# Performance work log

Hardware: AMD Instinct MI355X
Metric: run time of the kernel (lower is better)

## Reference

```python
import jax, jax.numpy as jnp
import numpy as np

B, N, DESC, H, MAXK = 32, 2048, 16, 64, 2
P = DESC + H            # concat feature dim
KMAT = 2 * MAXK + 1     # num diffusion matrices (identity + MAXK per support)


def setup_inputs() -> dict:
    key = jax.random.key(0)
    ks = jax.random.split(key, 8)
    return {
        "inputs": jax.random.normal(ks[0], (B, N * DESC), jnp.float32),
        "state": jax.random.normal(ks[1], (B, N * H), jnp.float32),
        "adj": jax.random.uniform(ks[2], (N, N), jnp.float32),
        "theta_r": jax.random.normal(ks[3], (P * KMAT, H), jnp.float32) * 0.05,
        "theta_u": jax.random.normal(ks[4], (P * KMAT, H), jnp.float32) * 0.05,
        "theta_c": jax.random.normal(ks[5], (P * KMAT, H), jnp.float32) * 0.05,
        "bias_r": jnp.zeros((1, H), jnp.float32),
        "bias_u": jnp.zeros((1, H), jnp.float32),
        "bias_c": jnp.zeros((1, H), jnp.float32),
    }


def _random_walk_T(adj):
    # transpose(D^-1 A): row-normalize then transpose
    d = jnp.sum(adj, axis=1, keepdims=True)
    d_inv = jnp.where(d > 0, 1.0 / d, 0.0)
    return (d_inv * adj).T  # [N, N]


def _gconv(x_in, h, supports, theta, bias):
    # x_in: [B, N*DESC], h: [B, N*H]
    x = jnp.concatenate(
        [x_in.reshape(B, N, DESC), h.reshape(B, N, H)], axis=-1
    )  # [B, N, P]
    xs = [x]
    for S in supports:
        xk = x
        for _ in range(MAXK):  # pure powers S^k x, as in the source
            xk = jnp.einsum("mn,bnp->bmp", S, xk)
            xs.append(xk)
    all_x = jnp.stack(xs, axis=-1)  # [B, N, P, KMAT]
    out = all_x.reshape(B * N, P * KMAT) @ theta + bias  # [B*N, H]
    return out.reshape(B, N * H)


def reference(inputs, state, adj, theta_r, theta_u, theta_c, bias_r, bias_u, bias_c):
    supports = (_random_walk_T(adj), _random_walk_T(adj.T))
    r = jax.nn.sigmoid(_gconv(inputs, state, supports, theta_r, bias_r))
    u = jax.nn.sigmoid(_gconv(inputs, state, supports, theta_u, bias_u))
    c = jnp.tanh(_gconv(inputs, r * state, supports, theta_c, bias_c))
    return u * state + (1.0 - u) * c  # [B, N*H]
```

## Files before the change

kernel.cpp:

```cpp
#include <hip/hip_runtime.h>
#include <hip/hip_bf16.h>

#define Bb    32
#define Nn_   2048
#define DESCn 16
#define Hn    64
#define Pn    80
#define KM    5

#define XSTRIDE ((size_t)Bb * Pn * Nn_)

typedef __attribute__((ext_vector_type(8))) short bf16x8;
typedef __attribute__((ext_vector_type(4))) short s16x4;
typedef __attribute__((ext_vector_type(4))) float f32x4;

__device__ __forceinline__ short f2bf(float f) {
    unsigned u = __builtin_bit_cast(unsigned, f);
    u = u + 0x7FFFu + ((u >> 16) & 1u);
    return (short)(u >> 16);
}
__device__ __forceinline__ float bf2f(short s) {
    unsigned u = ((unsigned)(unsigned short)s) << 16;
    return __builtin_bit_cast(float, u);
}

__device__ __forceinline__ void glds16(const void* g, void* l) {
    __builtin_amdgcn_global_load_lds((const __attribute__((address_space(1))) void*)g,
                                     (__attribute__((address_space(3))) void*)l, 16, 0, 0);
}


__global__ void sums_kernel(const float* __restrict__ adj, float* __restrict__ rsum,
                            float* __restrict__ csum) {
    __shared__ float tile[64][65];
    const int r0 = blockIdx.y * 64, c0 = blockIdx.x * 64;
    const int t = threadIdx.x;
    for (int i = t; i < 64 * 64; i += 256)
        tile[i >> 6][i & 63] = adj[(size_t)(r0 + (i >> 6)) * Nn_ + c0 + (i & 63)];
    __syncthreads();
    if (t < 64) {
        float s = 0.f;
#pragma unroll 8
        for (int j = 0; j < 64; ++j) s += tile[t][j];
        atomicAdd(&rsum[r0 + t], s);
    } else if (t < 128) {
        int c = t - 64;
        float s = 0.f;
#pragma unroll 8
        for (int j = 0; j < 64; ++j) s += tile[j][c];
        atomicAdd(&csum[c0 + c], s);
    }
}

__global__ void inv2_kernel(const float* __restrict__ rs, const float* __restrict__ cs,
                            float* __restrict__ ri, float* __restrict__ ci) {
    int i = blockIdx.x * 256 + threadIdx.x;
    if (i < Nn_) {
        ri[i] = rs[i] > 0.f ? 1.f / rs[i] : 0.f;
        ci[i] = cs[i] > 0.f ? 1.f / cs[i] : 0.f;
    }
}

__global__ void build_S_kernel(const float* __restrict__ adj, const float* __restrict__ rinv,
                               const float* __restrict__ cinv, short* __restrict__ S0,
                               short* __restrict__ S1, short* __restrict__ S0T,
                               short* __restrict__ S1T) {
    __shared__ float tile[64][65];
    int r0 = blockIdx.y * 64, c0 = blockIdx.x * 64;
    for (int i = threadIdx.x; i < 64 * 64; i += 256) {
        int r = i >> 6, c = i & 63;
        float a = adj[(size_t)(r0 + r) * Nn_ + c0 + c];
        size_t o = (size_t)(r0 + r) * Nn_ + c0 + c;
        S1[o]  = f2bf(a * cinv[c0 + c]);
        S0T[o] = f2bf(a * rinv[r0 + r]);
    }
    for (int i = threadIdx.x; i < 64 * 64; i += 256) {
        int a = i >> 6, b = i & 63;
        tile[a][b] = adj[(size_t)(c0 + a) * Nn_ + r0 + b];
    }
    __syncthreads();
    for (int i = threadIdx.x; i < 64 * 64; i += 256) {
        int r = i >> 6, c = i & 63;
        float at = tile[c][r];
        size_t o = (size_t)(r0 + r) * Nn_ + c0 + c;
        S0[o]  = f2bf(at * rinv[c0 + c]);
        S1T[o] = f2bf(at * cinv[r0 + r]);
    }
}


__global__ void build_x0_kernel(const float* __restrict__ inputs, const float* __restrict__ state,
                                short* __restrict__ x0) {
    const int b = blockIdx.y, n0 = blockIdx.x * 64;
    __shared__ float sIn[64][17];
    __shared__ float sSt[64][65];
    const int t = threadIdx.x;
    const float* ip = inputs + ((size_t)b * Nn_ + n0) * DESCn;
    for (int i = t; i < 64 * DESCn; i += 256) sIn[i >> 4][i & 15] = ip[i];
    const float* sp = state + ((size_t)b * Nn_ + n0) * Hn;
    for (int i = t; i < 64 * Hn; i += 256) sSt[i >> 6][i & 63] = sp[i];
    __syncthreads();
    for (int i = t; i < Pn * 64; i += 256) {
        int pp = i >> 6, nn = i & 63;
        float v = (pp < DESCn) ? sIn[nn][pp] : sSt[nn][pp - DESCn];
        x0[((size_t)pp * Bb + b) * Nn_ + n0 + nn] = f2bf(v);
    }
}

__global__ void reorder_theta3_kernel(const float* __restrict__ thR, const float* __restrict__ thU,
                                      const float* __restrict__ thC, short* __restrict__ TR,
                                      short* __restrict__ TU, short* __restrict__ TC) {
    int i = blockIdx.x * 256 + threadIdx.x;
    if (i >= KM * 64 * 96) return;
    int k = i / (64 * 96);
    int rem = i % (64 * 96);
    int h = rem / 96, pp = rem % 96;
    if (pp < Pn) {
        size_t idx = ((size_t)pp * KM + k) * Hn + h;
        TR[i] = f2bf(thR[idx]);
        TU[i] = f2bf(thU[idx]);
        TC[i] = f2bf(thC[idx]);
    } else {
        TR[i] = 0; TU[i] = 0; TC[i] = 0;
    }
}


struct GemmJob  { const short* A; const short* B; short* D; int yStart; };
struct GemmJobs { GemmJob j[4]; };

#define MMAQ(RH, CH, RB)                                                        \
    {                                                                           \
        __builtin_amdgcn_s_setprio(1);                                          \
        _Pragma("unroll")                                                       \
        for (int ks = 0; ks < 2; ++ks)                                          \
            _Pragma("unroll")                                                   \
            for (int fm = 0; fm < 4; ++fm)                                      \
                _Pragma("unroll")                                               \
                for (int fn = 0; fn < 2; ++fn)                                  \
                    acc[RH][CH][fm][fn] = __builtin_amdgcn_mfma_f32_16x16x32_bf16( \
                        rA[fm][ks], RB[fn][ks], acc[RH][CH][fm][fn], 0, 0, 0);  \
        __builtin_amdgcn_s_setprio(0);                                          \
    }

#define LOADA(D_, RH)                                                           \
    _Pragma("unroll")                                                           \
    for (int fm = 0; fm < 4; ++fm)                                              \
        _Pragma("unroll")                                                       \
        for (int ks = 0; ks < 2; ++ks)                                          \
            rA[fm][ks] = readA(D_, RH, fm, ks);

#define LOADB(D_, CH, RB)                                                       \
    _Pragma("unroll")                                                           \
    for (int fn = 0; fn < 2; ++fn)                                              \
        _Pragma("unroll")                                                       \
        for (int ks = 0; ks < 2; ++ks)                                          \
            RB[fn][ks] = readB(D_, CH, fn, ks);

__global__ __launch_bounds__(512, 2)
void gemm_bt_256(GemmJobs jobs, int nJobs, int K, int NN) {
    __shared__ __align__(16) short lds[65536];

    const int by = blockIdx.y;
    int jsel = 0;
#pragma unroll
    for (int q = 1; q < 4; ++q)
        if (q < nJobs && by >= jobs.j[q].yStart) jsel = q;
    const GemmJob jb = jobs.j[jsel];
    const short* __restrict__ A  = jb.A;
    const short* __restrict__ Bm = jb.B;
    short* __restrict__ D = jb.D;

    const int c0 = (by - jb.yStart) * 256;
    const int m0 = blockIdx.x * 256;
    const int tid = threadIdx.x;
    const int w = tid >> 6, lane = tid & 63;
    const int wm = w >> 2, wn = w & 3;
    const int l16 = lane & 15, g = lane >> 4;
    const int swz = l16 & 7;

    const int srow = tid >> 3;
    const int scol = ((tid & 7) ^ (srow & 7)) * 8;
    const int stOff = w * 512;

    const short* Abase = A + (size_t)c0 * K;
    const short* Bbase = Bm + (size_t)m0 * K;

    auto stageA = [&](int h, int t) {
        const short* gb = Abase + (size_t)(h * 128) * K + t * 64 + scol;
        short* lb = lds + ((t & 1) * 16384 + h * 8192) + stOff;
#pragma unroll
        for (int i = 0; i < 2; ++i)
            glds16(gb + (size_t)(i * 64 + srow) * K, lb + i * 4096);
    };
    auto stageB = [&](int h, int t) {
        const short* gb = Bbase + (size_t)(h * 128) * K + t * 64 + scol;
        short* lb = lds + (32768 + (t & 1) * 16384 + h * 8192) + stOff;
#pragma unroll
        for (int i = 0; i < 2; ++i)
            glds16(gb + (size_t)(i * 64 + srow) * K, lb + i * 4096);
    };

    auto readA = [&](int d, int rh, int fm, int ks) -> bf16x8 {
        int r7 = rh * 64 + fm * 16 + l16;
        int idx = d * 16384 + wm * 8192 + r7 * 64 + (((ks * 4 + g) ^ swz) * 8);
        return *(const bf16x8*)(lds + idx);
    };
    auto readB = [&](int d, int ch, int fn, int ks) -> bf16x8 {
        int r7 = (wn & 1) * 64 + ch * 32 + fn * 16 + l16;
        int idx = 32768 + d * 16384 + (wn >> 1) * 8192 + r7 * 64 + (((ks * 4 + g) ^ swz) * 8);
        return *(const bf16x8*)(lds + idx);
    };

    f32x4 acc[2][2][4][2];
    const f32x4 fz = {0.f, 0.f, 0.f, 0.f};
#pragma unroll
    for (int a = 0; a < 2; ++a)
#pragma unroll
        for (int b = 0; b < 2; ++b)
#pragma unroll
            for (int c = 0; c < 4; ++c)
#pragma unroll
                for (int d = 0; d < 2; ++d) acc[a][b][c][d] = fz;

    bf16x8 rA[4][2], rB0[2][2], rB1[2][2];

    const int KS = K >> 6;
    const int J  = KS >> 1;

    stageA(0, 0); stageA(1, 0); stageB(0, 0); stageB(1, 0);
    stageB(0, 1); stageB(1, 1);
    asm volatile("s_waitcnt vmcnt(4)" ::: "memory");
    __builtin_amdgcn_s_barrier();

#pragma unroll 1
    for (int j = 0; j < J; ++j) {
        const int t1  = 2 * j + 1;
        const int tn0 = (2 * j + 2 < KS) ? 2 * j + 2 : KS - 1;
        const int tn1 = (2 * j + 3 < KS) ? 2 * j + 3 : KS - 1;

        LOADA(0, 0); LOADB(0, 0, rB0);
        stageA(0, t1);
        __builtin_amdgcn_s_barrier();
        MMAQ(0, 0, rB0);
        __builtin_amdgcn_s_barrier();
        LOADB(0, 1, rB1);
        stageA(1, t1);
        __builtin_amdgcn_s_barrier();
        MMAQ(0, 1, rB1);
        __builtin_amdgcn_s_barrier();
        LOADA(0, 1);
        stageB(0, tn0);
        __builtin_amdgcn_s_barrier();
        MMAQ(1, 1, rB1);
        __builtin_amdgcn_s_barrier();
        stageB(1, tn0);
        asm volatile("s_waitcnt vmcnt(4)" ::: "memory");
        __builtin_amdgcn_s_barrier();
        MMAQ(1, 0, rB0);
        __builtin_amdgcn_s_barrier();
        LOADA(1, 0); LOADB(1, 0, rB0);
        stageA(0, tn0);
        __builtin_amdgcn_s_barrier();
        MMAQ(0, 0, rB0);
        __builtin_amdgcn_s_barrier();
        LOADB(1, 1, rB1);
        stageA(1, tn0);
        __builtin_amdgcn_s_barrier();
        MMAQ(0, 1, rB1);
        __builtin_amdgcn_s_barrier();
        LOADA(1, 1);
        stageB(0, tn1);
        __builtin_amdgcn_s_barrier();
        MMAQ(1, 1, rB1);
        __builtin_amdgcn_s_barrier();
        stageB(1, tn1);
        asm volatile("s_waitcnt vmcnt(4)" ::: "memory");
        __builtin_amdgcn_s_barrier();
        MMAQ(1, 0, rB0);
        __builtin_amdgcn_s_barrier();
    }

    asm volatile("s_waitcnt vmcnt(0)" ::: "memory");
    __syncthreads();
    float* tb = (float*)lds + w * 1088;
#pragma unroll
    for (int rh = 0; rh < 2; ++rh)
#pragma unroll
        for (int fm = 0; fm < 4; ++fm) {
#pragma unroll
            for (int ch = 0; ch < 2; ++ch)
#pragma unroll
                for (int fn = 0; fn < 2; ++fn) {
                    f32x4 v = acc[rh][ch][fm][fn];
#pragma unroll
                    for (int r = 0; r < 4; ++r)
                        tb[(g * 4 + r) * 68 + ch * 32 + fn * 16 + l16] = v[r];
                }
            const int crow0 = c0 + wm * 128 + rh * 64 + fm * 16;
            const int mcol = m0 + wn * 64 + lane;
#pragma unroll
            for (int rr = 0; rr < 16; ++rr)
                D[(size_t)(crow0 + rr) * NN + mcol] = f2bf(tb[rr * 68 + lane]);
        }
}


__global__ __launch_bounds__(256, 2)
void theta_ru_kernel(const short* __restrict__ X, const short* __restrict__ ThR,
                     const short* __restrict__ ThU, const float* __restrict__ biasR,
                     const float* __restrict__ biasU, const float* __restrict__ state,
                     short* __restrict__ Uout, short* __restrict__ x0) {
    __shared__ short ldsAr[64 * 40];
    __shared__ short ldsAu[64 * 40];
    __shared__ short ldsB[32 * 136];
    const int b = blockIdx.y, n0 = blockIdx.x * 128;
    const int t = threadIdx.x, w = t >> 6, lane = t & 63;
    const int l16 = lane & 15, g = lane >> 4;
    const f32x4 fz = {0.f, 0.f, 0.f, 0.f};
    const bf16x8 bz = {0, 0, 0, 0, 0, 0, 0, 0};

    f32x4 aR[4][2], aU[4][2];
#pragma unroll
    for (int i = 0; i < 4; i++)
#pragma unroll
        for (int j = 0; j < 2; j++) { aR[i][j] = fz; aU[i][j] = fz; }

    const int hA = t >> 2, pcA = (t & 3) * 8;

    for (int kb = 0; kb < KM; kb++) {
        for (int ks = 0; ks < 3; ks++) {
            __syncthreads();
            *(bf16x8*)(ldsAr + hA * 40 + pcA) =
                *(const bf16x8*)(ThR + ((size_t)kb * 64 + hA) * 96 + ks * 32 + pcA);
            *(bf16x8*)(ldsAu + hA * 40 + pcA) =
                *(const bf16x8*)(ThU + ((size_t)kb * 64 + hA) * 96 + ks * 32 + pcA);
#pragma unroll
            for (int i = 0; i < 2; i++) {
                int q = t + i * 256;
                int pp = q >> 4, nc = (q & 15) * 8;
                int pg = ks * 32 + pp;
                bf16x8 v = bz;
                if (pg < Pn)
                    v = *(const bf16x8*)(X + (size_t)kb * XSTRIDE + ((size_t)pg * Bb + b) * Nn_ + n0 + nc);
                *(bf16x8*)(ldsB + pp * 136 + nc) = v;
            }
            __syncthreads();
            bf16x8 ar[4], au[4];
#pragma unroll
            for (int mi = 0; mi < 4; mi++) {
                int hr = mi * 16 + l16;
                ar[mi] = *(const bf16x8*)(ldsAr + hr * 40 + g * 8);
                au[mi] = *(const bf16x8*)(ldsAu + hr * 40 + g * 8);
            }
#pragma unroll
            for (int nj = 0; nj < 2; nj++) {
                int col = w * 32 + nj * 16 + l16;
                bf16x8 bv;
#pragma unroll
                for (int j = 0; j < 8; j++) bv[j] = ldsB[(g * 8 + j) * 136 + col];
#pragma unroll
                for (int mi = 0; mi < 4; mi++) {
                    aR[mi][nj] = __builtin_amdgcn_mfma_f32_16x16x32_bf16(ar[mi], bv, aR[mi][nj], 0, 0, 0);
                    aU[mi][nj] = __builtin_amdgcn_mfma_f32_16x16x32_bf16(au[mi], bv, aU[mi][nj], 0, 0, 0);
                }
            }
        }
    }
#pragma unroll
    for (int mi = 0; mi < 4; mi++)
#pragma unroll
        for (int nj = 0; nj < 2; nj++) {
            int n = n0 + w * 32 + nj * 16 + l16;
            int h0 = mi * 16 + g * 4;
            size_t base = ((size_t)b * Nn_ + n) * Hn + h0;
            f32x4 st = *(const f32x4*)(state + base);
            s16x4 uv;
#pragma unroll
            for (int r = 0; r < 4; r++) {
                float zr = aR[mi][nj][r] + biasR[h0 + r];
                float zu = aU[mi][nj][r] + biasU[h0 + r];
                float rr = 1.f / (1.f + __expf(-zr));
                uv[r] = f2bf(1.f / (1.f + __expf(-zu)));
                x0[((size_t)(DESCn + h0 + r) * Bb + b) * Nn_ + n] = f2bf(rr * st[r]);
            }
            *(s16x4*)(Uout + base) = uv;
        }
}

__global__ __launch_bounds__(256, 2)
void theta_c_kernel(const short* __restrict__ X, const short* __restrict__ ThC,
                    const float* __restrict__ biasC, const short* __restrict__ U,
                    const float* __restrict__ state, float* __restrict__ out) {
    __shared__ short ldsA[64 * 40];
    __shared__ short ldsB[32 * 136];
    const int b = blockIdx.y, n0 = blockIdx.x * 128;
    const int t = threadIdx.x, w = t >> 6, lane = t & 63;
    const int l16 = lane & 15, g = lane >> 4;
    const f32x4 fz = {0.f, 0.f, 0.f, 0.f};
    const bf16x8 bz = {0, 0, 0, 0, 0, 0, 0, 0};

    f32x4 aC[4][2];
#pragma unroll
    for (int i = 0; i < 4; i++)
#pragma unroll
        for (int j = 0; j < 2; j++) aC[i][j] = fz;

    const int hA = t >> 2, pcA = (t & 3) * 8;

    for (int kb = 0; kb < KM; kb++) {
        for (int ks = 0; ks < 3; ks++) {
            __syncthreads();
            *(bf16x8*)(ldsA + hA * 40 + pcA) =
                *(const bf16x8*)(ThC + ((size_t)kb * 64 + hA) * 96 + ks * 32 + pcA);
#pragma unroll
            for (int i = 0; i < 2; i++) {
                int q = t + i * 256;
                int pp = q >> 4, nc = (q & 15) * 8;
                int pg = ks * 32 + pp;
                bf16x8 v = bz;
                if (pg < Pn)
                    v = *(const bf16x8*)(X + (size_t)kb * XSTRIDE + ((size_t)pg * Bb + b) * Nn_ + n0 + nc);
                *(bf16x8*)(ldsB + pp * 136 + nc) = v;
            }
            __syncthreads();
            bf16x8 ac[4];
#pragma unroll
            for (int mi = 0; mi < 4; mi++)
                ac[mi] = *(const bf16x8*)(ldsA + (mi * 16 + l16) * 40 + g * 8);
#pragma unroll
            for (int nj = 0; nj < 2; nj++) {
                int col = w * 32 + nj * 16 + l16;
                bf16x8 bv;
#pragma unroll
                for (int j = 0; j < 8; j++) bv[j] = ldsB[(g * 8 + j) * 136 + col];
#pragma unroll
                for (int mi = 0; mi < 4; mi++)
                    aC[mi][nj] = __builtin_amdgcn_mfma_f32_16x16x32_bf16(ac[mi], bv, aC[mi][nj], 0, 0, 0);
            }
        }
    }
#pragma unroll
    for (int mi = 0; mi < 4; mi++)
#pragma unroll
        for (int nj = 0; nj < 2; nj++) {
            int n = n0 + w * 32 + nj * 16 + l16;
            int h0 = mi * 16 + g * 4;
            size_t base = ((size_t)b * Nn_ + n) * Hn + h0;
            f32x4 st = *(const f32x4*)(state + base);
            s16x4 uv = *(const s16x4*)(U + base);
            f32x4 o;
#pragma unroll
            for (int r = 0; r < 4; r++) {
                float cc = tanhf(aC[mi][nj][r] + biasC[h0 + r]);
                float uu = bf2f(uv[r]);
                o[r] = uu * st[r] + (1.f - uu) * cc;
            }
            *(f32x4*)(out + base) = o;
        }
}


extern "C" void kernel_launch(void* const* d_in, const int* in_sizes, int n_in,
                              void* d_out, int out_size, void* d_ws, size_t ws_size,
                              hipStream_t stream) {
    (void)in_sizes; (void)n_in; (void)out_size; (void)ws_size;
    const float* inputs = (const float*)d_in[0];
    const float* state  = (const float*)d_in[1];
    const float* adj    = (const float*)d_in[2];
    const float* thR    = (const float*)d_in[3];
    const float* thU    = (const float*)d_in[4];
    const float* thC    = (const float*)d_in[5];
    const float* bR     = (const float*)d_in[6];
    const float* bU     = (const float*)d_in[7];
    const float* bC     = (const float*)d_in[8];
    float* out = (float*)d_out;

    char* p = (char*)d_ws;
    auto alloc = [&](size_t bytes) -> void* {
        void* r = (void*)p;
        p += (bytes + 255) & ~(size_t)255;
        return r;
    };
    short* S0   = (short*)alloc((size_t)Nn_ * Nn_ * 2);
    short* S1   = (short*)alloc((size_t)Nn_ * Nn_ * 2);
    short* Ssq0 = (short*)alloc((size_t)Nn_ * Nn_ * 2);
    short* Ssq1 = (short*)alloc((size_t)Nn_ * Nn_ * 2);
    float* rinv = (float*)alloc(Nn_ * 4);
    float* cinv = (float*)alloc(Nn_ * 4);
    float* sums = (float*)alloc(2 * Nn_ * 4);
    short* xb   = (short*)alloc(5 * XSTRIDE * 2);
    short* TR   = (short*)alloc((size_t)KM * 64 * 96 * 2);
    short* TU   = (short*)alloc((size_t)KM * 64 * 96 * 2);
    short* TC   = (short*)alloc((size_t)KM * 64 * 96 * 2);
    short* Ub   = (short*)alloc((size_t)Bb * Nn_ * Hn * 2);

    short* x0 = xb;
    short* y1 = xb + 1 * XSTRIDE;
    short* y2 = xb + 2 * XSTRIDE;
    short* y3 = xb + 3 * XSTRIDE;
    short* y4 = xb + 4 * XSTRIDE;
    short* S0T = y3;
    short* S1T = y4;
    const size_t HOFF = (size_t)DESCn * Bb * Nn_;

    hipMemsetAsync(sums, 0, 2 * Nn_ * 4, stream);
    sums_kernel<<<dim3(32, 32), 256, 0, stream>>>(adj, sums, sums + Nn_);
    inv2_kernel<<<Nn_ / 256, 256, 0, stream>>>(sums, sums + Nn_, rinv, cinv);
    build_S_kernel<<<dim3(32, 32), 256, 0, stream>>>(adj, rinv, cinv, S0, S1, S0T, S1T);
    build_x0_kernel<<<dim3(32, Bb), 256, 0, stream>>>(inputs, state, x0);
    int rt_grid = (KM * 64 * 96 + 255) / 256;
    reorder_theta3_kernel<<<rt_grid, 256, 0, stream>>>(thR, thU, thC, TR, TU, TC);

    GemmJobs d1;
    d1.j[0] = { S0, S0T, Ssq0, 0 };
    d1.j[1] = { S1, S1T, Ssq1, 8 };
    d1.j[2] = { x0, S0,   y1, 16 };
    d1.j[3] = d1.j[2];
    gemm_bt_256<<<dim3(8, 26), 512, 0, stream>>>(d1, 3, Nn_, Nn_);

    GemmJobs d2;
    d2.j[0] = { x0, S1,   y3, 0 };
    d2.j[1] = { x0, Ssq0, y2, 10 };
    d2.j[2] = { x0, Ssq1, y4, 20 };
    d2.j[3] = d2.j[2];
    gemm_bt_256<<<dim3(8, 30), 512, 0, stream>>>(d2, 3, Nn_, Nn_);

    theta_ru_kernel<<<dim3(Nn_ / 128, Bb), 256, 0, stream>>>(xb, TR, TU, bR, bU, state, Ub, x0);

    GemmJobs d3;
    d3.j[0] = { x0 + HOFF, S0,   y1 + HOFF, 0 };
    d3.j[1] = { x0 + HOFF, Ssq0, y2 + HOFF, 8 };
    d3.j[2] = { x0 + HOFF, S1,   y3 + HOFF, 16 };
    d3.j[3] = { x0 + HOFF, Ssq1, y4 + HOFF, 24 };
    gemm_bt_256<<<dim3(8, 32), 512, 0, stream>>>(d3, 4, Nn_, Nn_);

    theta_c_kernel<<<dim3(Nn_ / 128, Bb), 256, 0, stream>>>(xb, TC, bC, Ub, state, out);
}
```

Before: 266.1 us.

## Cut GEMM main-loop barriers from sixteen to four per iteration

Restructures the ping-pong main loop of the 256x256 bf16 GEMM so each half-stage loads A and both B fragments up front, issues both stage copies together, then runs two MMA quads before a single barrier. Explicit lgkmcnt waits and sched_barriers keep the compiler from moving LDS reads across the fewer sync points. The aim is to remove barrier stalls and wave-interleaving overhead. In exchange it raises register pressure by holding more fragments live and loses the fine-grained barrier interleaving that gave priority-based overlap between the two waves per SIMD.

Result: faster. 259.9 us (-2.3%).

```diff
diff --git a/kernel.cpp b/kernel.cpp
--- a/kernel.cpp
+++ b/kernel.cpp
@@ -157,6 +157,19 @@
         for (int ks = 0; ks < 2; ++ks)                                          \
             RB[fn][ks] = readB(D_, CH, fn, ks);
 
+#define SYNCW()                                                   \
+    asm volatile("s_waitcnt lgkmcnt(0)" ::: "memory");            \
+    __builtin_amdgcn_sched_barrier(0);                            \
+    __builtin_amdgcn_s_barrier();                                 \
+    __builtin_amdgcn_sched_barrier(0);
+
+#define SYNCWV()                                                  \
+    asm volatile("s_waitcnt lgkmcnt(0)" ::: "memory");            \
+    __builtin_amdgcn_sched_barrier(0);                            \
+    asm volatile("s_waitcnt vmcnt(4)" ::: "memory");              \
+    __builtin_amdgcn_s_barrier();                                 \
+    __builtin_amdgcn_sched_barrier(0);
+
 __global__ __launch_bounds__(512, 2)
 void gemm_bt_256(GemmJobs jobs, int nJobs, int K, int NN) {
     __shared__ __align__(16) short lds[65536];
@@ -232,6 +245,7 @@
     stageB(0, 1); stageB(1, 1);
     asm volatile("s_waitcnt vmcnt(4)" ::: "memory");
     __builtin_amdgcn_s_barrier();
+    __builtin_amdgcn_sched_barrier(0);
 
 #pragma unroll 1
     for (int j = 0; j < J; ++j) {
@@ -239,46 +253,30 @@
         const int tn0 = (2 * j + 2 < KS) ? 2 * j + 2 : KS - 1;
         const int tn1 = (2 * j + 3 < KS) ? 2 * j + 3 : KS - 1;
 
-        LOADA(0, 0); LOADB(0, 0, rB0);
-        stageA(0, t1);
-        __builtin_amdgcn_s_barrier();
+        LOADA(0, 0);
+        LOADB(0, 0, rB0);
+        LOADB(0, 1, rB1);
+        stageA(0, t1); stageA(1, t1);
         MMAQ(0, 0, rB0);
-        __builtin_amdgcn_s_barrier();
-        LOADB(0, 1, rB1);
-        stageA(1, t1);
-        __builtin_amdgcn_s_barrier();
         MMAQ(0, 1, rB1);
-        __builtin_amdgcn_s_barrier();
+        SYNCW();
         LOADA(0, 1);
-        stageB(0, tn0);
-        __builtin_amdgcn_s_barrier();
+        stageB(0, tn0); stageB(1, tn0);
         MMAQ(1, 1, rB1);
-        __builtin_amdgcn_s_barrier();
-        stageB(1, tn0);
-        asm volatile("s_waitcnt vmcnt(4)" ::: "memory");
-        __builtin_amdgcn_s_barrier();
         MMAQ(1, 0, rB0);
-        __builtin_amdgcn_s_barrier();
-        LOADA(1, 0); LOADB(1, 0, rB0);
-        stageA(0, tn0);
-        __builtin_amdgcn_s_barrier();
+        SYNCWV();
+        LOADA(1, 0);
+        LOADB(1, 0, rB0);
+        LOADB(1, 1, rB1);
+        stageA(0, tn0); stageA(1, tn0);
         MMAQ(0, 0, rB0);
-        __builtin_amdgcn_s_barrier();
-        LOADB(1, 1, rB1);
-        stageA(1, tn0);
-        __builtin_amdgcn_s_barrier();
         MMAQ(0, 1, rB1);
-        __builtin_amdgcn_s_barrier();
+        SYNCW();
         LOADA(1, 1);
-        stageB(0, tn1);
-        __builtin_amdgcn_s_barrier();
+        stageB(0, tn1); stageB(1, tn1);
         MMAQ(1, 1, rB1);
-        __builtin_amdgcn_s_barrier();
-        stageB(1, tn1);
-        asm volatile("s_waitcnt vmcnt(4)" ::: "memory");
-        __builtin_amdgcn_s_barrier();
         MMAQ(1, 0, rB0);
-        __builtin_amdgcn_s_barrier();
+        SYNCWV();
     }
 
     asm volatile("s_waitcnt vmcnt(0)" ::: "memory");
```
